# Kernel optimization log

Hardware: AMD Instinct MI355X
Metric: run time of the kernel (lower is better)

## Reference

```python
import jax, jax.numpy as jnp
import numpy as np

B, N, C = 2, 5000, 768
H, D = 12, 64
E = 160000
NEG_SLOPE = 0.2


def setup_inputs() -> dict:
    key = jax.random.key(0)
    ks = jax.random.split(key, 6)
    x = jax.random.normal(ks[0], (B, N, C), dtype=jnp.float32)
    W = jax.random.normal(ks[1], (C, H * D), dtype=jnp.float32) * 0.02
    att_src = jax.random.normal(ks[2], (H, D), dtype=jnp.float32) * 0.1
    att_dst = jax.random.normal(ks[3], (H, D), dtype=jnp.float32) * 0.1
    bias = jnp.zeros((H * D,), dtype=jnp.float32)
    edge_index = jax.random.randint(ks[4], (2, E), 0, N, dtype=jnp.int32)
    return {"x": x, "W": W, "att_src": att_src, "att_dst": att_dst,
            "bias": bias, "edge_index": edge_index}


def reference(x, W, att_src, att_dst, bias, edge_index):
    # Batched GATConv with shared edge_index (PyG defaults: self-loops,
    # leaky_relu(0.2), per-dst softmax, concat heads, bias).
    loops = jnp.arange(N, dtype=edge_index.dtype)
    src = jnp.concatenate([edge_index[0], loops])  # [Etot]
    dst = jnp.concatenate([edge_index[1], loops])

    h = (x @ W).reshape(B, N, H, D)                        # [B,N,H,D]
    a_src = jnp.einsum('bnhd,hd->bnh', h, att_src)         # [B,N,H]
    a_dst = jnp.einsum('bnhd,hd->bnh', h, att_dst)

    e = jax.nn.leaky_relu(a_src[:, src] + a_dst[:, dst], NEG_SLOPE)  # [B,Etot,H]
    e = jnp.moveaxis(e, 1, 0)                              # [Etot,B,H]

    # numerically stable softmax over edges grouped by destination node
    m = jax.ops.segment_max(e, dst, num_segments=N)        # [N,B,H]
    ex = jnp.exp(e - m[dst])
    denom = jax.ops.segment_sum(ex, dst, num_segments=N)   # [N,B,H]
    alpha = ex / (denom[dst] + 1e-16)                      # [Etot,B,H]

    h_src = jnp.moveaxis(h[:, src], 1, 0)                  # [Etot,B,H,D]
    msg = alpha[..., None] * h_src
    out = jax.ops.segment_sum(msg, dst, num_segments=N)    # [N,B,H,D]
    out = jnp.moveaxis(out, 0, 1).reshape(B, N, H * D) + bias
    return out
```

## Files before the change

### kernel.cpp

```cpp
#include <hip/hip_runtime.h>

#define Bv 2
#define Nv 5000
#define Cv 768
#define Hv 12
#define Dv 64
#define Ev 160000
#define ETOT (Ev + Nv)
#define HD 768
#define NEG 0.2f
#define Mv (Bv * Nv)
#define MPAD 10240
#define DEGMAX 128
#define DEGPAD 136
#define DEGW 132

typedef __bf16 bf16x8 __attribute__((ext_vector_type(8)));
typedef float f32x4 __attribute__((ext_vector_type(4)));

#define GLD16(gsrc, ldst)                                                      \
  __builtin_amdgcn_global_load_lds(                                            \
      (const __attribute__((address_space(1))) unsigned int*)(gsrc),           \
      (__attribute__((address_space(3))) unsigned int*)(ldst), 16, 0, 0)

__device__ __forceinline__ unsigned short f2b(float f) {
  unsigned u = __float_as_uint(f);
  return (unsigned short)((u + 0x7FFFu + ((u >> 16) & 1u)) >> 16);
}

#define NB_CVTX 3840
#define NB_CVTW 576
#define NB_CNT  645
__global__ __launch_bounds__(256) void k_prep(const float* __restrict__ x,
                                              unsigned short* __restrict__ xb,
                                              const float* __restrict__ W,
                                              unsigned short* __restrict__ Wt,
                                              const int* __restrict__ ei,
                                              int* __restrict__ cnt,
                                              int* __restrict__ csrp) {
  const int blk = blockIdx.x;
  const int t = threadIdx.x;
  if (blk < NB_CVTX) {
    size_t i = ((size_t)blk * 256 + t) * 8;
    unsigned short o[8];
    if (i < (size_t)Mv * Cv) {
      float4 v0 = *(const float4*)(x + i);
      float4 v1 = *(const float4*)(x + i + 4);
      o[0] = f2b(v0.x); o[1] = f2b(v0.y); o[2] = f2b(v0.z); o[3] = f2b(v0.w);
      o[4] = f2b(v1.x); o[5] = f2b(v1.y); o[6] = f2b(v1.z); o[7] = f2b(v1.w);
    } else {
      for (int j = 0; j < 8; ++j) o[j] = 0;
    }
    *(uint4*)(xb + i) = *(const uint4*)o;
  } else if (blk < NB_CVTX + NB_CVTW) {
    __shared__ float s[32][33];
    const int bw = blk - NB_CVTX;
    const int n0 = (bw % 24) * 32, k0 = (bw / 24) * 32;
    const int tx = t & 31, ty = t >> 5;
#pragma unroll
    for (int i = 0; i < 4; ++i)
      s[ty + i * 8][tx] = W[(size_t)(k0 + ty + i * 8) * HD + n0 + tx];
    __syncthreads();
#pragma unroll
    for (int i = 0; i < 4; ++i)
      Wt[(size_t)(n0 + ty + i * 8) * Cv + k0 + tx] = f2b(s[tx][ty + i * 8]);
  } else {
    const int e = (blk - NB_CVTX - NB_CVTW) * 256 + t;
    if (e < ETOT) {
      int dst = (e < Ev) ? ei[Ev + e] : (e - Ev);
      int src = (e < Ev) ? ei[e] : (e - Ev);
      int pos = atomicAdd(&cnt[dst], 1);
      csrp[dst * DEGMAX + pos] = src;
    }
  }
}

#define STAGE(bi, kk)                                                          \
  {                                                                            \
    _Pragma("unroll")                                                          \
    for (int i = 0; i < 4; ++i) {                                              \
      const int r = i * 64 + rs;                                               \
      GLD16(A + (size_t)(bm + r) * Cv + (kk) + sl * 8, &As[bi][t * 8 + i * 4096]); \
    }                                                                          \
    _Pragma("unroll")                                                          \
    for (int i = 0; i < 2; ++i) {                                              \
      const int r = i * 64 + rs;                                               \
      GLD16(Bt + (size_t)(bn + r) * Cv + (kk) + sl * 8, &Bs[bi][t * 8 + i * 4096]); \
    }                                                                          \
  }

__global__ __launch_bounds__(512) void k_gemm_mfma(const unsigned short* __restrict__ A,
                                                   const unsigned short* __restrict__ Bt,
                                                   unsigned short* __restrict__ C,
                                                   const float* __restrict__ att_src,
                                                   const float* __restrict__ att_dst,
                                                   float* __restrict__ asrc,
                                                   float* __restrict__ adst) {
  __shared__ unsigned short As[2][256 * 64];
  __shared__ unsigned short Bs[2][128 * 64];
  const int l0 = blockIdx.x;
  const int xcd = l0 & 7, j = l0 >> 3;
  const int bm = (xcd + 8 * (j / 6)) * 256;
  const int bn = (j % 6) * 128;
  const int t = threadIdx.x;
  const int w = t >> 6, l = t & 63;
  const int wr = w >> 1, wc = w & 1;
  const int g = l >> 4, li = l & 15;
  f32x4 acc[4][4] = {};

  const int rs = t >> 3;
  const int sl = (t & 7) ^ (rs & 7);

  STAGE(0, 0);
  __syncthreads();
  int cur = 0;
#pragma unroll 1
  for (int step = 0; step < Cv / 64; ++step) {
    if (step + 1 < Cv / 64) STAGE(cur ^ 1, (step + 1) * 64);
#pragma unroll
    for (int ks = 0; ks < 2; ++ks) {
      bf16x8 a[4], b[4];
#pragma unroll
      for (int mi = 0; mi < 4; ++mi) {
        const int row = wr * 64 + mi * 16 + li;
        const int slot = (ks * 4 + g) ^ (row & 7);
        a[mi] = *(const bf16x8*)&As[cur][row * 64 + slot * 8];
      }
#pragma unroll
      for (int nj = 0; nj < 4; ++nj) {
        const int row = wc * 64 + nj * 16 + li;
        const int slot = (ks * 4 + g) ^ (row & 7);
        b[nj] = *(const bf16x8*)&Bs[cur][row * 64 + slot * 8];
      }
#pragma unroll
      for (int mi = 0; mi < 4; ++mi)
#pragma unroll
        for (int nj = 0; nj < 4; ++nj)
          acc[mi][nj] = __builtin_amdgcn_mfma_f32_16x16x32_bf16(a[mi], b[nj], acc[mi][nj], 0, 0, 0);
    }
    __syncthreads();
    cur ^= 1;
  }
#pragma unroll
  for (int mi = 0; mi < 4; ++mi) {
#pragma unroll
    for (int nj = 0; nj < 4; ++nj) {
      const int col = bn + wc * 64 + nj * 16 + li;
#pragma unroll
      for (int r4 = 0; r4 < 4; ++r4) {
        const int row = bm + wr * 64 + mi * 16 + g * 4 + r4;
        C[(size_t)row * HD + col] = f2b(acc[mi][nj][r4]);
      }
    }
  }
  {
    const int head = (bn >> 6) + wc;
    float aS[4], aD[4];
#pragma unroll
    for (int nj = 0; nj < 4; ++nj) {
      aS[nj] = att_src[head * Dv + nj * 16 + li];
      aD[nj] = att_dst[head * Dv + nj * 16 + li];
    }
#pragma unroll
    for (int mi = 0; mi < 4; ++mi) {
#pragma unroll
      for (int r4 = 0; r4 < 4; ++r4) {
        float vs = 0.f, vd = 0.f;
#pragma unroll
        for (int nj = 0; nj < 4; ++nj) {
          const float hv = acc[mi][nj][r4];
          vs = fmaf(hv, aS[nj], vs);
          vd = fmaf(hv, aD[nj], vd);
        }
        vs += __shfl_xor(vs, 1); vd += __shfl_xor(vd, 1);
        vs += __shfl_xor(vs, 2); vd += __shfl_xor(vd, 2);
        vs += __shfl_xor(vs, 4); vd += __shfl_xor(vd, 4);
        vs += __shfl_xor(vs, 8); vd += __shfl_xor(vd, 8);
        const int row = bm + wr * 64 + mi * 16 + g * 4 + r4;
        if (li == 0 && row < Mv) {
          asrc[(size_t)row * Hv + head] = vs;
          adst[(size_t)row * Hv + head] = vd;
        }
      }
    }
  }
}

#define EDGE_FMA(c, wv)                                              \
  {                                                                  \
    acc[0] = fmaf(wv, __uint_as_float((c).x << 16), acc[0]);         \
    acc[1] = fmaf(wv, __uint_as_float((c).x & 0xFFFF0000u), acc[1]); \
    acc[2] = fmaf(wv, __uint_as_float((c).y << 16), acc[2]);         \
    acc[3] = fmaf(wv, __uint_as_float((c).y & 0xFFFF0000u), acc[3]); \
    acc[4] = fmaf(wv, __uint_as_float((c).z << 16), acc[4]);         \
    acc[5] = fmaf(wv, __uint_as_float((c).z & 0xFFFF0000u), acc[5]); \
    acc[6] = fmaf(wv, __uint_as_float((c).w << 16), acc[6]);         \
    acc[7] = fmaf(wv, __uint_as_float((c).w & 0xFFFF0000u), acc[7]); \
  }

__global__ __launch_bounds__(192) void k_agg(const unsigned short* __restrict__ h2,
                                             const int* __restrict__ cnt,
                                             const int* __restrict__ csrp,
                                             const float* __restrict__ asrc,
                                             const float* __restrict__ adst,
                                             const float* __restrict__ bias,
                                             float* __restrict__ out) {
  const int xcd = blockIdx.x & 7;
  const int idx = blockIdx.x >> 3;
  const int b = xcd >> 2;
  const int pair = (xcd & 3) * 625 + idx;
  const int n0 = pair * 2;
  const int t = threadIdx.x;
  __shared__ int s_src[2][DEGPAD];
  __shared__ float s_w[2][Hv][DEGW];
  __shared__ float s_inv[2][16];
  const int d0 = cnt[n0], d1 = cnt[n0 + 1];
  for (int i = t; i < 2 * DEGPAD; i += 192) {
    const int jn = i >= DEGPAD;
    const int ii = i - jn * DEGPAD;
    const int dd = jn ? d1 : d0;
    int sv = 0;
    if (ii < dd) sv = csrp[(n0 + jn) * DEGMAX + ii];
    s_src[jn][ii] = sv;
  }
  __syncthreads();
  {
    const int jn = t / 96, rq = t % 96;
    const int q = rq >> 5, slot = rq & 31;
    const int deg = jn ? d1 : d0;
    const int degp = (deg + 7) & ~7;
    const f32x4 adv4 = *(const f32x4*)&adst[((size_t)b * Nv + n0 + jn) * Hv + q * 4];
    f32x4 ps = {0.f, 0.f, 0.f, 0.f};
    for (int i = slot; i < deg; i += 32) {
      const int src = s_src[jn][i];
      const f32x4 as4 = *(const f32x4*)&asrc[((size_t)b * Nv + src) * Hv + q * 4];
#pragma unroll
      for (int jq = 0; jq < 4; ++jq) {
        float v = as4[jq] + adv4[jq];
        v = fmaxf(v, NEG * v);
        float ex = __expf(v);
        s_w[jn][q * 4 + jq][i] = ex;
        ps[jq] += ex;
      }
    }
    for (int i = deg + slot; i < degp; i += 32) {
#pragma unroll
      for (int jq = 0; jq < 4; ++jq) s_w[jn][q * 4 + jq][i] = 0.f;
    }
#pragma unroll
    for (int jq = 0; jq < 4; ++jq) {
      ps[jq] += __shfl_xor(ps[jq], 1);
      ps[jq] += __shfl_xor(ps[jq], 2);
      ps[jq] += __shfl_xor(ps[jq], 4);
      ps[jq] += __shfl_xor(ps[jq], 8);
      ps[jq] += __shfl_xor(ps[jq], 16);
    }
    if (slot == 0) {
      f32x4 inv;
#pragma unroll
      for (int jq = 0; jq < 4; ++jq) inv[jq] = 1.0f / (ps[jq] + 1e-16f);
      *(f32x4*)&s_inv[jn][q * 4] = inv;
    }
  }
  __syncthreads();
  const int jn = t >= 96;
  const int tl = t - jn * 96;
  const int hl = tl >> 3;
  const int degp = ((jn ? d1 : d0) + 7) & ~7;
  float acc[8] = {};
  const unsigned short* hrow = h2 + (size_t)b * Nv * HD + tl * 8;
  uint4 cA[4], cB[4];
#pragma unroll
  for (int k = 0; k < 4; ++k)
    cA[k] = *(const uint4*)(hrow + (size_t)s_src[jn][k] * HD);
  for (int base = 0; base < degp; base += 8) {
#pragma unroll
    for (int k = 0; k < 4; ++k)
      cB[k] = *(const uint4*)(hrow + (size_t)s_src[jn][base + 4 + k] * HD);
    {
      const f32x4 w4 = *(const f32x4*)&s_w[jn][hl][base];
      EDGE_FMA(cA[0], w4[0]); EDGE_FMA(cA[1], w4[1]);
      EDGE_FMA(cA[2], w4[2]); EDGE_FMA(cA[3], w4[3]);
    }
#pragma unroll
    for (int k = 0; k < 4; ++k)
      cA[k] = *(const uint4*)(hrow + (size_t)s_src[jn][base + 8 + k] * HD);
    {
      const f32x4 w4 = *(const f32x4*)&s_w[jn][hl][base + 4];
      EDGE_FMA(cB[0], w4[0]); EDGE_FMA(cB[1], w4[1]);
      EDGE_FMA(cB[2], w4[2]); EDGE_FMA(cB[3], w4[3]);
    }
  }
  const float invh = s_inv[jn][hl];
  const int od = tl * 8;
  float4 o0, o1;
  o0.x = fmaf(acc[0], invh, bias[od + 0]);
  o0.y = fmaf(acc[1], invh, bias[od + 1]);
  o0.z = fmaf(acc[2], invh, bias[od + 2]);
  o0.w = fmaf(acc[3], invh, bias[od + 3]);
  o1.x = fmaf(acc[4], invh, bias[od + 4]);
  o1.y = fmaf(acc[5], invh, bias[od + 5]);
  o1.z = fmaf(acc[6], invh, bias[od + 6]);
  o1.w = fmaf(acc[7], invh, bias[od + 7]);
  float* op = out + ((size_t)b * Nv + n0 + jn) * HD + od;
  *(float4*)op = o0;
  *(float4*)(op + 4) = o1;
}

extern "C" void kernel_launch(void* const* d_in, const int* in_sizes, int n_in,
                              void* d_out, int out_size, void* d_ws, size_t ws_size,
                              hipStream_t stream) {
  const float* x = (const float*)d_in[0];
  const float* W = (const float*)d_in[1];
  const float* att_src = (const float*)d_in[2];
  const float* att_dst = (const float*)d_in[3];
  const float* bias = (const float*)d_in[4];
  const int* ei = (const int*)d_in[5];
  float* out = (float*)d_out;

  unsigned short* h2 = (unsigned short*)d_ws;
  unsigned short* xbf = h2 + (size_t)MPAD * HD;
  unsigned short* wt = xbf + (size_t)MPAD * HD;
  float* asrc = (float*)(wt + (size_t)HD * Cv);
  float* adst = asrc + (size_t)Bv * Nv * Hv;
  int* cnt = (int*)(adst + (size_t)Bv * Nv * Hv);
  int* csrp = cnt + Nv;

  hipMemsetAsync(cnt, 0, sizeof(int) * Nv, stream);

  k_prep<<<NB_CVTX + NB_CVTW + NB_CNT, 256, 0, stream>>>(x, xbf, W, wt, ei, cnt, csrp);
  k_gemm_mfma<<<240, 512, 0, stream>>>(xbf, wt, h2, att_src, att_dst, asrc, adst);
  k_agg<<<Bv * Nv / 2, 192, 0, stream>>>(h2, cnt, csrp, asrc, adst, bias, out);
}
```

Measured before the change: 97.54 us.

## Fuse fp32-to-bf16 conversion of x into GEMM staging and merge CSR scatter blocks

```diff
diff --git a/kernel.cpp b/kernel.cpp
--- a/kernel.cpp
+++ b/kernel.cpp
@@ -28,34 +28,15 @@
   return (unsigned short)((u + 0x7FFFu + ((u >> 16) & 1u)) >> 16);
 }
 
-#define NB_CVTX 3840
 #define NB_CVTW 576
-#define NB_CNT  645
-__global__ __launch_bounds__(256) void k_prep(const float* __restrict__ x,
-                                              unsigned short* __restrict__ xb,
-                                              const float* __restrict__ W,
-                                              unsigned short* __restrict__ Wt,
-                                              const int* __restrict__ ei,
-                                              int* __restrict__ cnt,
-                                              int* __restrict__ csrp) {
+__global__ __launch_bounds__(256) void k_pre(const float* __restrict__ W,
+                                             unsigned short* __restrict__ Wt,
+                                             int* __restrict__ cnt) {
   const int blk = blockIdx.x;
   const int t = threadIdx.x;
-  if (blk < NB_CVTX) {
-    size_t i = ((size_t)blk * 256 + t) * 8;
-    unsigned short o[8];
-    if (i < (size_t)Mv * Cv) {
-      float4 v0 = *(const float4*)(x + i);
-      float4 v1 = *(const float4*)(x + i + 4);
-      o[0] = f2b(v0.x); o[1] = f2b(v0.y); o[2] = f2b(v0.z); o[3] = f2b(v0.w);
-      o[4] = f2b(v1.x); o[5] = f2b(v1.y); o[6] = f2b(v1.z); o[7] = f2b(v1.w);
-    } else {
-      for (int j = 0; j < 8; ++j) o[j] = 0;
-    }
-    *(uint4*)(xb + i) = *(const uint4*)o;
-  } else if (blk < NB_CVTX + NB_CVTW) {
+  if (blk < NB_CVTW) {
     __shared__ float s[32][33];
-    const int bw = blk - NB_CVTX;
-    const int n0 = (bw % 24) * 32, k0 = (bw / 24) * 32;
+    const int n0 = (blk % 24) * 32, k0 = (blk / 24) * 32;
     const int tx = t & 31, ty = t >> 5;
 #pragma unroll
     for (int i = 0; i < 4; ++i)
@@ -65,42 +46,70 @@
     for (int i = 0; i < 4; ++i)
       Wt[(size_t)(n0 + ty + i * 8) * Cv + k0 + tx] = f2b(s[tx][ty + i * 8]);
   } else {
-    const int e = (blk - NB_CVTX - NB_CVTW) * 256 + t;
+    for (int i = t; i < Nv; i += 256) cnt[i] = 0;
+  }
+}
+
+#define NB_GEMM 480
+#define NB_SCAT ((ETOT + 255) / 256)
+#define STAGEG(bi, kk)                                                         \
+  {                                                                            \
+    _Pragma("unroll")                                                          \
+    for (int i = 0; i < 4; ++i) {                                              \
+      const int r = i * 32 + rs;                                               \
+      GLD16(Bt + (size_t)(bn + r) * Cv + (kk) + sl * 8, &Bs[bi][t * 8 + i * 2048]); \
+    }                                                                          \
+    float4 av[4][2];                                                           \
+    _Pragma("unroll")                                                          \
+    for (int i = 0; i < 4; ++i) {                                              \
+      const int grow = bm + i * 32 + rs;                                       \
+      if (grow < Mv) {                                                         \
+        const float* ap = Ax + (size_t)grow * Cv + (kk) + ssl * 8;             \
+        av[i][0] = *(const float4*)ap;                                         \
+        av[i][1] = *(const float4*)(ap + 4);                                   \
+      } else {                                                                 \
+        av[i][0] = make_float4(0.f, 0.f, 0.f, 0.f);                            \
+        av[i][1] = av[i][0];                                                   \
+      }                                                                        \
+    }                                                                          \
+    _Pragma("unroll")                                                          \
+    for (int i = 0; i < 4; ++i) {                                              \
+      const int r = i * 32 + rs;                                               \
+      unsigned short o[8];                                                     \
+      o[0] = f2b(av[i][0].x); o[1] = f2b(av[i][0].y);                          \
+      o[2] = f2b(av[i][0].z); o[3] = f2b(av[i][0].w);                          \
+      o[4] = f2b(av[i][1].x); o[5] = f2b(av[i][1].y);                          \
+      o[6] = f2b(av[i][1].z); o[7] = f2b(av[i][1].w);                          \
+      const int ds = ssl ^ (r & 7);                                            \
+      *(uint4*)&As[bi][r * 64 + ds * 8] = *(const uint4*)o;                    \
+    }                                                                          \
+  }
+
+__global__ __launch_bounds__(256) void k_gemm_sc(const float* __restrict__ Ax,
+                                                 const unsigned short* __restrict__ Bt,
+                                                 unsigned short* __restrict__ C,
+                                                 const float* __restrict__ att_src,
+                                                 const float* __restrict__ att_dst,
+                                                 float* __restrict__ asrc,
+                                                 float* __restrict__ adst,
+                                                 const int* __restrict__ ei,
+                                                 int* __restrict__ cnt,
+                                                 int* __restrict__ csrp) {
+  if (blockIdx.x >= NB_GEMM) {
+    const int e = (blockIdx.x - NB_GEMM) * 256 + threadIdx.x;
     if (e < ETOT) {
       int dst = (e < Ev) ? ei[Ev + e] : (e - Ev);
       int src = (e < Ev) ? ei[e] : (e - Ev);
       int pos = atomicAdd(&cnt[dst], 1);
       csrp[dst * DEGMAX + pos] = src;
     }
-  }
-}
-
-#define STAGE(bi, kk)                                                          \
-  {                                                                            \
-    _Pragma("unroll")                                                          \
-    for (int i = 0; i < 4; ++i) {                                              \
-      const int r = i * 64 + rs;                                               \
-      GLD16(A + (size_t)(bm + r) * Cv + (kk) + sl * 8, &As[bi][t * 8 + i * 4096]); \
-    }                                                                          \
-    _Pragma("unroll")                                                          \
-    for (int i = 0; i < 2; ++i) {                                              \
-      const int r = i * 64 + rs;                                               \
-      GLD16(Bt + (size_t)(bn + r) * Cv + (kk) + sl * 8, &Bs[bi][t * 8 + i * 4096]); \
-    }                                                                          \
-  }
-
-__global__ __launch_bounds__(512) void k_gemm_mfma(const unsigned short* __restrict__ A,
-                                                   const unsigned short* __restrict__ Bt,
-                                                   unsigned short* __restrict__ C,
-                                                   const float* __restrict__ att_src,
-                                                   const float* __restrict__ att_dst,
-                                                   float* __restrict__ asrc,
-                                                   float* __restrict__ adst) {
-  __shared__ unsigned short As[2][256 * 64];
+    return;
+  }
+  __shared__ unsigned short As[2][128 * 64];
   __shared__ unsigned short Bs[2][128 * 64];
   const int l0 = blockIdx.x;
   const int xcd = l0 & 7, j = l0 >> 3;
-  const int bm = (xcd + 8 * (j / 6)) * 256;
+  const int bm = (xcd + 8 * (j / 6)) * 128;
   const int bn = (j % 6) * 128;
   const int t = threadIdx.x;
   const int w = t >> 6, l = t & 63;
@@ -109,14 +118,15 @@
   f32x4 acc[4][4] = {};
 
   const int rs = t >> 3;
-  const int sl = (t & 7) ^ (rs & 7);
-
-  STAGE(0, 0);
+  const int ssl = t & 7;
+  const int sl = ssl ^ (rs & 7);
+
+  STAGEG(0, 0);
   __syncthreads();
   int cur = 0;
 #pragma unroll 1
   for (int step = 0; step < Cv / 64; ++step) {
-    if (step + 1 < Cv / 64) STAGE(cur ^ 1, (step + 1) * 64);
+    if (step + 1 < Cv / 64) STAGEG(cur ^ 1, (step + 1) * 64);
 #pragma unroll
     for (int ks = 0; ks < 2; ++ks) {
       bf16x8 a[4], b[4];
@@ -319,16 +329,14 @@
   float* out = (float*)d_out;
 
   unsigned short* h2 = (unsigned short*)d_ws;
-  unsigned short* xbf = h2 + (size_t)MPAD * HD;
-  unsigned short* wt = xbf + (size_t)MPAD * HD;
+  unsigned short* wt = h2 + (size_t)MPAD * HD;
   float* asrc = (float*)(wt + (size_t)HD * Cv);
   float* adst = asrc + (size_t)Bv * Nv * Hv;
   int* cnt = (int*)(adst + (size_t)Bv * Nv * Hv);
   int* csrp = cnt + Nv;
 
-  hipMemsetAsync(cnt, 0, sizeof(int) * Nv, stream);
-
-  k_prep<<<NB_CVTX + NB_CVTW + NB_CNT, 256, 0, stream>>>(x, xbf, W, wt, ei, cnt, csrp);
-  k_gemm_mfma<<<240, 512, 0, stream>>>(xbf, wt, h2, att_src, att_dst, asrc, adst);
+  k_pre<<<NB_CVTW + 1, 256, 0, stream>>>(W, wt, cnt);
+  k_gemm_sc<<<NB_GEMM + NB_SCAT, 256, 0, stream>>>(x, wt, h2, att_src, att_dst,
+                                                   asrc, adst, ei, cnt, csrp);
   k_agg<<<Bv * Nv / 2, 192, 0, stream>>>(h2, cnt, csrp, asrc, adst, bias, out);
 }
```

Measured after the change: 83.56 us, median of 2. 14.3% less time.
